# Optimization experiments

Hardware: AMD Instinct MI355X
Metric: run time of the kernel (lower is better)

The kernel has to match this reference:

```python
import jax, jax.numpy as jnp
import numpy as np

N, D, G, HID, GDIM, TAIL = 1048576, 128, 4096, 50, 201, 33  # TAIL = ec50_dim + 1


def setup_inputs() -> dict:
    key = jax.random.key(0)
    ks = jax.random.split(key, 8)
    x = jax.random.normal(ks[0], (N, D), dtype=jnp.float32)
    batch = jnp.sort(jax.random.randint(ks[1], (N,), 0, G))
    edge_index = jax.random.randint(ks[2], (2, 4096), 0, N)
    edge_attr = jax.random.normal(ks[3], (4096, 8), dtype=jnp.float32)
    u = jax.random.normal(ks[4], (G, 64), dtype=jnp.float32)
    W1 = jax.random.normal(ks[5], (4 * D, HID), dtype=jnp.float32) / np.float32(np.sqrt(4 * D))
    b1 = jnp.zeros((HID,), jnp.float32)
    ln_g = jnp.ones((HID,), jnp.float32)
    ln_b = jnp.zeros((HID,), jnp.float32)
    W2 = jax.random.normal(ks[6], (HID, GDIM), dtype=jnp.float32) / np.float32(np.sqrt(HID))
    b2 = jnp.zeros((GDIM,), jnp.float32)
    return {"x": x, "edge_index": edge_index, "edge_attr": edge_attr, "u": u,
            "batch": batch, "W1": W1, "b1": b1, "ln_g": ln_g, "ln_b": ln_b,
            "W2": W2, "b2": b2}


def _multi_aggr(x, batch, num_segments):
    # mean / std / max / min segment reductions, concatenated on feature dim.
    cnt = jax.ops.segment_sum(jnp.ones((x.shape[0],), x.dtype), batch, num_segments)
    cnt = jnp.maximum(cnt, 1.0)[:, None]
    s = jax.ops.segment_sum(x, batch, num_segments)
    s2 = jax.ops.segment_sum(x * x, batch, num_segments)
    mean = s / cnt
    var = s2 / cnt - mean * mean
    std = jnp.sqrt(jax.nn.relu(var) + 1e-5)  # PyG StdAggregation semantics
    mx = jax.ops.segment_max(x, batch, num_segments)
    mn = jax.ops.segment_min(x, batch, num_segments)
    return jnp.concatenate([mean, std, mx, mn], axis=1)  # [G, 4*D]


def _layer_norm(h, g, b, eps=1e-5):
    mu = jnp.mean(h, axis=-1, keepdims=True)
    var = jnp.mean((h - mu) ** 2, axis=-1, keepdims=True)
    return (h - mu) * jax.lax.rsqrt(var + eps) * g + b


def reference(x, edge_index, edge_attr, u, batch, W1, b1, ln_g, ln_b, W2, b2):
    num_segments = u.shape[0]
    aggr = _multi_aggr(x, batch, num_segments)           # [G, 4*D]
    h = jax.nn.selu(aggr @ W1 + b1)                       # Linear + SELU
    h = _layer_norm(h, ln_g, ln_b)                        # LayerNorm(hidden)
    head = h @ W2 + b2                                    # [G, g_dim]
    tail = u[:, -TAIL:]                                   # [G, 33]
    return jnp.concatenate([head, tail], axis=1)          # [G, 234]
```

## Files before the change

### kernel.cpp

```cpp
#include <hip/hip_runtime.h>

#define N_ROWS 1048576
#define DIM    128
#define G_SEG  4096
#define HID    50
#define GDIM_  201
#define TAILN  33
#define OUTW   (GDIM_ + TAILN)
#define U_COLS 64

__global__ void seg_starts_kernel(const int* __restrict__ batch, int* __restrict__ start, int n) {
    int i = blockIdx.x * blockDim.x + threadIdx.x;
    if (i >= n) return;
    int b = batch[i];
    if (i == 0) {
        for (int g = 0; g <= b; ++g) start[g] = 0;
    } else {
        int bp = batch[i - 1];
        for (int g = bp + 1; g <= b; ++g) start[g] = i;
    }
    if (i == n - 1) {
        for (int g = b + 1; g <= G_SEG; ++g) start[g] = n;
    }
}

__launch_bounds__(256)
__global__ void pna_main_kernel(const float* __restrict__ x,
                                const float* __restrict__ u,
                                const int*   __restrict__ start,
                                const float* __restrict__ W1,
                                const float* __restrict__ b1,
                                const float* __restrict__ lng,
                                const float* __restrict__ lnb,
                                const float* __restrict__ W2,
                                const float* __restrict__ b2,
                                float* __restrict__ out) {
    __shared__ float red[8][128];
    __shared__ float aggr[512];
    __shared__ float part[4][HID];
    __shared__ float hbuf[HID];
    __shared__ float hn[HID];

    const int g  = blockIdx.x;
    const int t  = threadIdx.x;
    const int fg = t & 31;
    const int rg = t >> 5;
    const int r0 = start[g];
    const int r1 = start[g + 1];
    const int cnt = r1 - r0;

    float s[4], s2[4], mx[4], mn[4];
#pragma unroll
    for (int j = 0; j < 4; ++j) { s[j] = 0.f; s2[j] = 0.f; mx[j] = -INFINITY; mn[j] = INFINITY; }

    const int fbase = fg * 4;
    for (int r = r0 + rg; r < r1; r += 8) {
        float4 v = *reinterpret_cast<const float4*>(x + (size_t)r * DIM + fbase);
        float f[4] = {v.x, v.y, v.z, v.w};
#pragma unroll
        for (int j = 0; j < 4; ++j) {
            s[j]  += f[j];
            s2[j]  = fmaf(f[j], f[j], s2[j]);
            mx[j]  = fmaxf(mx[j], f[j]);
            mn[j]  = fminf(mn[j], f[j]);
        }
    }

    const float inv_c = 1.0f / (float)((cnt > 1) ? cnt : 1);

#pragma unroll
    for (int j = 0; j < 4; ++j) red[rg][fbase + j] = s[j];
    __syncthreads();
    if (t < 128) {
        float a = red[0][t];
#pragma unroll
        for (int k = 1; k < 8; ++k) a += red[k][t];
        aggr[t] = a * inv_c;
    }
    __syncthreads();
#pragma unroll
    for (int j = 0; j < 4; ++j) red[rg][fbase + j] = s2[j];
    __syncthreads();
    if (t < 128) {
        float a = red[0][t];
#pragma unroll
        for (int k = 1; k < 8; ++k) a += red[k][t];
        float mean = aggr[t];
        float var  = a * inv_c - mean * mean;
        var = fmaxf(var, 0.0f);
        aggr[128 + t] = sqrtf(var + 1e-5f);
    }
    __syncthreads();
#pragma unroll
    for (int j = 0; j < 4; ++j) red[rg][fbase + j] = mx[j];
    __syncthreads();
    if (t < 128) {
        float a = red[0][t];
#pragma unroll
        for (int k = 1; k < 8; ++k) a = fmaxf(a, red[k][t]);
        aggr[256 + t] = a;
    }
    __syncthreads();
#pragma unroll
    for (int j = 0; j < 4; ++j) red[rg][fbase + j] = mn[j];
    __syncthreads();
    if (t < 128) {
        float a = red[0][t];
#pragma unroll
        for (int k = 1; k < 8; ++k) a = fminf(a, red[k][t]);
        aggr[384 + t] = a;
    }
    __syncthreads();

    if (t < 4 * HID) {
        const int q = t / HID;
        const int j = t - q * HID;
        const int k0 = q * 128;
        float acc = 0.f;
#pragma unroll 8
        for (int k = 0; k < 128; ++k) {
            acc = fmaf(aggr[k0 + k], W1[(size_t)(k0 + k) * HID + j], acc);
        }
        part[q][j] = acc;
    }
    __syncthreads();
    if (t < HID) {
        float acc = part[0][t] + part[1][t] + part[2][t] + part[3][t] + b1[t];
        float v = acc > 0.f ? acc : 1.6732632423543772f * expm1f(acc);
        hbuf[t] = 1.0507009873554805f * v;
    }
    __syncthreads();
    if (t < HID) {
        float mu = 0.f;
#pragma unroll
        for (int j2 = 0; j2 < HID; ++j2) mu += hbuf[j2];
        mu *= (1.0f / HID);
        float va = 0.f;
#pragma unroll
        for (int j2 = 0; j2 < HID; ++j2) { float d = hbuf[j2] - mu; va = fmaf(d, d, va); }
        va *= (1.0f / HID);
        hn[t] = (hbuf[t] - mu) * rsqrtf(va + 1e-5f) * lng[t] + lnb[t];
    }
    __syncthreads();
    if (t < GDIM_) {
        float acc = b2[t];
#pragma unroll
        for (int j2 = 0; j2 < HID; ++j2) {
            acc = fmaf(hn[j2], W2[(size_t)j2 * GDIM_ + t], acc);
        }
        out[(size_t)g * OUTW + t] = acc;
    }
    if (t >= 201 && t < 201 + TAILN) {
        int i2 = t - 201;
        out[(size_t)g * OUTW + GDIM_ + i2] = u[(size_t)g * U_COLS + (U_COLS - TAILN) + i2];
    }
}

extern "C" void kernel_launch(void* const* d_in, const int* in_sizes, int n_in,
                              void* d_out, int out_size, void* d_ws, size_t ws_size,
                              hipStream_t stream) {
    const float* x     = (const float*)d_in[0];
    const float* u     = (const float*)d_in[3];
    const int*   batch = (const int*)d_in[4];
    const float* W1    = (const float*)d_in[5];
    const float* b1    = (const float*)d_in[6];
    const float* lng   = (const float*)d_in[7];
    const float* lnb   = (const float*)d_in[8];
    const float* W2    = (const float*)d_in[9];
    const float* b2    = (const float*)d_in[10];
    float* out = (float*)d_out;
    int* start = (int*)d_ws;

    seg_starts_kernel<<<N_ROWS / 256, 256, 0, stream>>>(batch, start, N_ROWS);
    pna_main_kernel<<<G_SEG, 256, 0, stream>>>(x, u, start, W1, b1, lng, lnb, W2, b2, out);
}
```

Measured before the change: 721.7 us.

## Replace segment-start kernel with in-kernel binary search; unroll nontemporal loads

```diff
diff --git a/kernel.cpp b/kernel.cpp
--- a/kernel.cpp
+++ b/kernel.cpp
@@ -9,25 +9,21 @@
 #define OUTW   (GDIM_ + TAILN)
 #define U_COLS 64
 
-__global__ void seg_starts_kernel(const int* __restrict__ batch, int* __restrict__ start, int n) {
-    int i = blockIdx.x * blockDim.x + threadIdx.x;
-    if (i >= n) return;
-    int b = batch[i];
-    if (i == 0) {
-        for (int g = 0; g <= b; ++g) start[g] = 0;
-    } else {
-        int bp = batch[i - 1];
-        for (int g = bp + 1; g <= b; ++g) start[g] = i;
+typedef float f4 __attribute__((ext_vector_type(4)));
+
+__device__ __forceinline__ int lower_bound_i(const int* __restrict__ a, int n, int key) {
+    int lo = 0, hi = n;
+    while (lo < hi) {
+        int mid = (lo + hi) >> 1;
+        if (a[mid] < key) lo = mid + 1; else hi = mid;
     }
-    if (i == n - 1) {
-        for (int g = b + 1; g <= G_SEG; ++g) start[g] = n;
-    }
+    return lo;
 }
 
 __launch_bounds__(256)
 __global__ void pna_main_kernel(const float* __restrict__ x,
                                 const float* __restrict__ u,
-                                const int*   __restrict__ start,
+                                const int*   __restrict__ batch,
                                 const float* __restrict__ W1,
                                 const float* __restrict__ b1,
                                 const float* __restrict__ lng,
@@ -45,8 +41,9 @@
     const int t  = threadIdx.x;
     const int fg = t & 31;
     const int rg = t >> 5;
-    const int r0 = start[g];
-    const int r1 = start[g + 1];
+
+    const int r0 = lower_bound_i(batch, N_ROWS, g);
+    const int r1 = lower_bound_i(batch, N_ROWS, g + 1);
     const int cnt = r1 - r0;
 
     float s[4], s2[4], mx[4], mn[4];
@@ -54,22 +51,36 @@
     for (int j = 0; j < 4; ++j) { s[j] = 0.f; s2[j] = 0.f; mx[j] = -INFINITY; mn[j] = INFINITY; }
 
     const int fbase = fg * 4;
-    for (int r = r0 + rg; r < r1; r += 8) {
-        float4 v = *reinterpret_cast<const float4*>(x + (size_t)r * DIM + fbase);
-        float f[4] = {v.x, v.y, v.z, v.w};
+    int r = r0 + rg;
+    for (; r + 8 < r1; r += 16) {
+        f4 va = __builtin_nontemporal_load(reinterpret_cast<const f4*>(x + (size_t)r * DIM + fbase));
+        f4 vb = __builtin_nontemporal_load(reinterpret_cast<const f4*>(x + (size_t)(r + 8) * DIM + fbase));
+        float fa[4] = {va.x, va.y, va.z, va.w};
+        float fb[4] = {vb.x, vb.y, vb.z, vb.w};
 #pragma unroll
         for (int j = 0; j < 4; ++j) {
-            s[j]  += f[j];
-            s2[j]  = fmaf(f[j], f[j], s2[j]);
-            mx[j]  = fmaxf(mx[j], f[j]);
-            mn[j]  = fminf(mn[j], f[j]);
+            s[j] += fa[j];  s2[j] = fmaf(fa[j], fa[j], s2[j]);
+            mx[j] = fmaxf(mx[j], fa[j]);  mn[j] = fminf(mn[j], fa[j]);
+        }
+#pragma unroll
+        for (int j = 0; j < 4; ++j) {
+            s[j] += fb[j];  s2[j] = fmaf(fb[j], fb[j], s2[j]);
+            mx[j] = fmaxf(mx[j], fb[j]);  mn[j] = fminf(mn[j], fb[j]);
+        }
+    }
+    if (r < r1) {
+        f4 va = __builtin_nontemporal_load(reinterpret_cast<const f4*>(x + (size_t)r * DIM + fbase));
+        float fa[4] = {va.x, va.y, va.z, va.w};
+#pragma unroll
+        for (int j = 0; j < 4; ++j) {
+            s[j] += fa[j];  s2[j] = fmaf(fa[j], fa[j], s2[j]);
+            mx[j] = fmaxf(mx[j], fa[j]);  mn[j] = fminf(mn[j], fa[j]);
         }
     }
 
     const float inv_c = 1.0f / (float)((cnt > 1) ? cnt : 1);
 
-#pragma unroll
-    for (int j = 0; j < 4; ++j) red[rg][fbase + j] = s[j];
+    *reinterpret_cast<float4*>(&red[rg][fbase]) = make_float4(s[0], s[1], s[2], s[3]);
     __syncthreads();
     if (t < 128) {
         float a = red[0][t];
@@ -78,8 +89,7 @@
         aggr[t] = a * inv_c;
     }
     __syncthreads();
-#pragma unroll
-    for (int j = 0; j < 4; ++j) red[rg][fbase + j] = s2[j];
+    *reinterpret_cast<float4*>(&red[rg][fbase]) = make_float4(s2[0], s2[1], s2[2], s2[3]);
     __syncthreads();
     if (t < 128) {
         float a = red[0][t];
@@ -91,8 +101,7 @@
         aggr[128 + t] = sqrtf(var + 1e-5f);
     }
     __syncthreads();
-#pragma unroll
-    for (int j = 0; j < 4; ++j) red[rg][fbase + j] = mx[j];
+    *reinterpret_cast<float4*>(&red[rg][fbase]) = make_float4(mx[0], mx[1], mx[2], mx[3]);
     __syncthreads();
     if (t < 128) {
         float a = red[0][t];
@@ -101,8 +110,7 @@
         aggr[256 + t] = a;
     }
     __syncthreads();
-#pragma unroll
-    for (int j = 0; j < 4; ++j) red[rg][fbase + j] = mn[j];
+    *reinterpret_cast<float4*>(&red[rg][fbase]) = make_float4(mn[0], mn[1], mn[2], mn[3]);
     __syncthreads();
     if (t < 128) {
         float a = red[0][t];
@@ -169,8 +177,6 @@
     const float* W2    = (const float*)d_in[9];
     const float* b2    = (const float*)d_in[10];
     float* out = (float*)d_out;
-    int* start = (int*)d_ws;
 
-    seg_starts_kernel<<<N_ROWS / 256, 256, 0, stream>>>(batch, start, N_ROWS);
-    pna_main_kernel<<<G_SEG, 256, 0, stream>>>(x, u, start, W1, b1, lng, lnb, W2, b2, out);
+    pna_main_kernel<<<G_SEG, 256, 0, stream>>>(x, u, batch, W1, b1, lng, lnb, W2, b2, out);
 }
```

Result: faster. 706.1 us (-2.2%).
